# Kernel optimization log

Hardware: AMD Instinct MI355X
Metric: run time of the kernel (lower is better)

Reference implementation:

```python
import jax, jax.numpy as jnp
import numpy as np

N_PEP, N_MHC, N_TCR = 20000, 5000, 100000
EMB, HID = 128, 256
E_PM, E_MT = 200000, 400000
B = 50000


def setup_inputs() -> dict:
    key = jax.random.key(0)
    ks = jax.random.split(key, 30)
    f32 = jnp.float32

    def w(k, shape, fan_in):
        # torch Linear default: U(-1/sqrt(fan_in), 1/sqrt(fan_in))
        lim = 1.0 / np.sqrt(fan_in)
        return jax.random.uniform(k, shape, dtype=f32, minval=-lim, maxval=lim)

    inp = {
        # embedding tables (learned params)
        "emb_pep": jax.random.normal(ks[0], (N_PEP, EMB), dtype=f32),
        "emb_mhc": jax.random.normal(ks[1], (N_MHC, EMB), dtype=f32),
        "emb_tcr": jax.random.normal(ks[2], (N_TCR, EMB), dtype=f32),
        # edge lists (src=edge_index[0], dst=edge_index[1])
        "src_pm": jax.random.randint(ks[3], (E_PM,), 0, N_PEP, dtype=jnp.int32),
        "dst_pm": jax.random.randint(ks[4], (E_PM,), 0, N_MHC, dtype=jnp.int32),
        "src_mt": jax.random.randint(ks[5], (E_MT,), 0, N_MHC, dtype=jnp.int32),
        "dst_mt": jax.random.randint(ks[6], (E_MT,), 0, N_TCR, dtype=jnp.int32),
        # triplet pack indices
        "pack_pep": jax.random.randint(ks[7], (B,), 0, N_PEP, dtype=jnp.int32),
        "pack_mhc": jax.random.randint(ks[8], (B,), 0, N_MHC, dtype=jnp.int32),
        "pack_tcr": jax.random.randint(ks[9], (B,), 0, N_TCR, dtype=jnp.int32),
        # SAGEConv params: Wl (aggregated neighbors, with bias), Wr (root, no bias)
        # layer 1: pep->mhc (src 128, dst 128); mhc->tcr (src 128, dst 128)
        "l1_pm_Wl": w(ks[10], (HID, EMB), EMB), "l1_pm_bl": w(ks[11], (HID,), EMB),
        "l1_pm_Wr": w(ks[12], (HID, EMB), EMB),
        "l1_mt_Wl": w(ks[13], (HID, EMB), EMB), "l1_mt_bl": w(ks[14], (HID,), EMB),
        "l1_mt_Wr": w(ks[15], (HID, EMB), EMB),
        # layer 2: pep->mhc (src 128, dst 256); mhc->tcr (src 256, dst 256)
        "l2_pm_Wl": w(ks[16], (HID, EMB), EMB), "l2_pm_bl": w(ks[17], (HID,), EMB),
        "l2_pm_Wr": w(ks[18], (HID, HID), HID),
        "l2_mt_Wl": w(ks[19], (HID, HID), HID), "l2_mt_bl": w(ks[20], (HID,), HID),
        "l2_mt_Wr": w(ks[21], (HID, HID), HID),
        # proj_pep and head MLP
        "proj_W": w(ks[22], (HID, EMB), EMB), "proj_b": w(ks[23], (HID,), EMB),
        "head_W1": w(ks[24], (HID, 3 * HID), 3 * HID), "head_b1": w(ks[25], (HID,), 3 * HID),
        "head_W2": w(ks[26], (1, HID), HID), "head_b2": w(ks[27], (1,), HID),
    }
    return inp


def _sage(x_src, x_dst, src, dst, Wl, bl, Wr, n_dst):
    # SAGEConv(mean): lin_l(mean_{j in N(i)} x_src[j]) + lin_r(x_dst[i])
    msg = jax.ops.segment_sum(x_src[src], dst, num_segments=n_dst)  # [n_dst, d_src]
    cnt = jax.ops.segment_sum(jnp.ones((src.shape[0],), x_src.dtype), dst, num_segments=n_dst)
    mean = msg / jnp.maximum(cnt, 1.0)[:, None]
    return mean @ Wl.T + bl + x_dst @ Wr.T


def reference(emb_pep, emb_mhc, emb_tcr,
              src_pm, dst_pm, src_mt, dst_mt,
              pack_pep, pack_mhc, pack_tcr,
              l1_pm_Wl, l1_pm_bl, l1_pm_Wr, l1_mt_Wl, l1_mt_bl, l1_mt_Wr,
              l2_pm_Wl, l2_pm_bl, l2_pm_Wr, l2_mt_Wl, l2_mt_bl, l2_mt_Wr,
              proj_W, proj_b, head_W1, head_b1, head_W2, head_b2):
    relu = jax.nn.relu
    # layer 1 (HeteroConv reads all relations from the same input dict)
    mhc1 = relu(_sage(emb_pep, emb_mhc, src_pm, dst_pm, l1_pm_Wl, l1_pm_bl, l1_pm_Wr, N_MHC))
    tcr1 = relu(_sage(emb_mhc, emb_tcr, src_mt, dst_mt, l1_mt_Wl, l1_mt_bl, l1_mt_Wr, N_TCR))
    # layer 2 ('pep' is never a destination, so it keeps its embedding)
    mhc2 = relu(_sage(emb_pep, mhc1, src_pm, dst_pm, l2_pm_Wl, l2_pm_bl, l2_pm_Wr, N_MHC))
    tcr2 = relu(_sage(mhc1, tcr1, src_mt, dst_mt, l2_mt_Wl, l2_mt_bl, l2_mt_Wr, N_TCR))
    # projections + triplet gather (dropout disabled: inference)
    hp = (emb_pep @ proj_W.T + proj_b)[pack_pep]  # [B, HID]
    hm = mhc2[pack_mhc]
    ht = tcr2[pack_tcr]
    z = jnp.concatenate([hp, hm, ht], axis=-1)  # [B, 3*HID]
    hidden = relu(z @ head_W1.T + head_b1)
    logits = hidden @ head_W2.T + head_b2
    return logits.squeeze(-1)
```

## Files before the change

kernel.cpp:

```cpp
#include <hip/hip_runtime.h>

constexpr int NPEP = 20000, NMHC = 5000, NTCR = 100000;
constexpr int EPM = 200000, EMT = 400000, BB = 50000;
constexpr int MAXU = 50000;

typedef __attribute__((ext_vector_type(8))) short bf16x8;
typedef __attribute__((ext_vector_type(4))) float f32x4;

__device__ inline ushort f2bf(float x) {
    union { float f; unsigned u; } v; v.f = x;
    unsigned r = (v.u + 0x7FFF + ((v.u >> 16) & 1)) >> 16;
    return (ushort)r;
}
__device__ inline float bf2f(ushort b) {
    union { unsigned u; float f; } t; t.u = ((unsigned)b) << 16; return t.f;
}
__device__ inline void bf2x2(unsigned u, float& a, float& b) {
    union { unsigned x; float f; } t1, t2;
    t1.x = u << 16; t2.x = u & 0xffff0000u;
    a = t1.f; b = t2.f;
}
__device__ inline ushort4 f4bf(float4 v) {
    return make_ushort4(f2bf(v.x), f2bf(v.y), f2bf(v.z), f2bf(v.w));
}

__global__ __launch_bounds__(256) void prep_kernel(
    int* __restrict__ ibz,
    const float4* __restrict__ emb_pep, ushort4* __restrict__ emb_pep_b,
    const float4* __restrict__ Wr1f, ushort4* __restrict__ Wr1_b,
    const float4* __restrict__ Wr2f, ushort4* __restrict__ Wr2_b,
    const float* __restrict__ head_W1, ushort4* __restrict__ W1b_b, ushort4* __restrict__ W1c_b,
    const float* __restrict__ l1_pm_Wl, const float* __restrict__ l1_pm_Wr,
    const float* __restrict__ l1_mt_Wl, ushort* __restrict__ Wcat1_b,
    const float* __restrict__ l2_pm_Wl, const float* __restrict__ l2_pm_Wr,
    const float* __restrict__ l2_mt_Wl, ushort* __restrict__ Wcat2_b,
    const float4* __restrict__ emb_mhc, ushort* __restrict__ Acat1,
    const float* __restrict__ proj_W, const float* __restrict__ proj_b,
    ushort* __restrict__ Wcomp_b, float* __restrict__ bp) {
    __shared__ float red[128];
    const int b = blockIdx.x, tid = threadIdx.x;
    if (b < 303) {
        int i = b * 256 + tid;
        if (i < 77500) ((int4*)ibz)[i] = make_int4(0, 0, 0, 0);
    } else if (b < 2803) {
        int i = (b - 303) * 256 + tid;
        if (i < 640000) emb_pep_b[i] = f4bf(emb_pep[i]);
    } else if (b < 2835) {
        int i = (b - 2803) * 256 + tid;
        if (i < 8192) Wr1_b[i] = f4bf(Wr1f[i]);
    } else if (b < 2899) {
        int i = (b - 2835) * 256 + tid;
        if (i < 16384) Wr2_b[i] = f4bf(Wr2f[i]);
    } else if (b < 2963) {
        int i = (b - 2899) * 256 + tid;
        if (i < 16384) {
            int n = i >> 6, k4 = (i & 63) * 4;
            float4 v = *(const float4*)(head_W1 + (size_t)n * 768 + 256 + k4);
            W1b_b[i] = f4bf(v);
        }
    } else if (b < 3027) {
        int i = (b - 2963) * 256 + tid;
        if (i < 16384) {
            int n = i >> 6, k4 = (i & 63) * 4;
            float4 v = *(const float4*)(head_W1 + (size_t)n * 768 + 512 + k4);
            W1c_b[i] = f4bf(v);
        }
    } else if (b < 3539) {
        int idx = (b - 3027) * 256 + tid;
        if (idx < 131072) {
            int r = idx >> 8, k = idx & 255;
            float v;
            if (r < 256) v = (k < 128) ? l1_pm_Wl[r * 128 + k] : l1_pm_Wr[r * 128 + (k - 128)];
            else         v = (k < 128) ? 0.f : l1_mt_Wl[(r - 256) * 128 + (k - 128)];
            Wcat1_b[idx] = f2bf(v);
        }
    } else if (b < 4307) {
        int idx = (b - 3539) * 256 + tid;
        if (idx < 196608) {
            int r = idx / 384, k = idx - r * 384;
            float v;
            if (r < 256) v = (k < 128) ? l2_pm_Wl[r * 128 + k] : l2_pm_Wr[r * 256 + (k - 128)];
            else         v = (k < 128) ? 0.f : l2_mt_Wl[(r - 256) * 256 + (k - 128)];
            Wcat2_b[idx] = f2bf(v);
        }
    } else if (b < 4932) {
        int i4 = (b - 4307) * 256 + tid;
        if (i4 < 160000) {
            int r = i4 >> 5, c4 = (i4 & 31) * 4;
            *(ushort4*)(Acat1 + (size_t)r * 256 + 128 + c4) = f4bf(emb_mhc[i4]);
        }
    } else {
        int i = b - 4932;
        const float* w1row = head_W1 + (size_t)i * 768;
        if (tid < 128) {
            float acc = 0.f;
            for (int k = 0; k < 256; k++) acc += w1row[k] * proj_W[k * 128 + tid];
            Wcomp_b[i * 128 + tid] = f2bf(acc);
            float pb = w1row[2 * tid] * proj_b[2 * tid] + w1row[2 * tid + 1] * proj_b[2 * tid + 1];
            red[tid] = pb;
        }
        __syncthreads();
        if (tid < 64) { red[tid] += red[tid + 64]; }
        __syncthreads();
        if (tid < 32) { red[tid] += red[tid + 32]; }
        __syncthreads();
        if (tid == 0) {
            float s = 0.f;
            for (int j = 0; j < 32; j++) s += red[j];
            bp[i] = s;
        }
    }
}

__global__ void hist2_kernel(const int* __restrict__ dst_pm, const int* __restrict__ dst_mt,
                             const int* __restrict__ pack_tcr,
                             int* __restrict__ deg_pm, int* __restrict__ deg_mt,
                             int* __restrict__ mark) {
    int t = blockIdx.x * blockDim.x + threadIdx.x;
    if (t < EPM) atomicAdd(&deg_pm[dst_pm[t]], 1);
    else if (t < EPM + EMT) atomicAdd(&deg_mt[dst_mt[t - EPM]], 1);
    else if (t < EPM + EMT + BB) mark[pack_tcr[t - EPM - EMT]] = 1;
}

__global__ __launch_bounds__(256) void blocksum2_kernel(const int* __restrict__ deg_pm,
                                                        const int* __restrict__ deg_mt,
                                                        const int* __restrict__ mark,
                                                        int* __restrict__ bsum_pm,
                                                        int* __restrict__ bsum_mt,
                                                        int* __restrict__ bsum_mk) {
    __shared__ int red[256];
    const int tid = threadIdx.x;
    const int* deg; int n, bi; int* bsum;
    if (blockIdx.x < 5) { deg = deg_pm; n = NMHC; bi = blockIdx.x; bsum = bsum_pm; }
    else if (blockIdx.x < 103) { deg = deg_mt; n = NTCR; bi = blockIdx.x - 5; bsum = bsum_mt; }
    else { deg = mark; n = NTCR; bi = blockIdx.x - 103; bsum = bsum_mk; }
    const int base = bi * 1024;
    int s = 0;
#pragma unroll
    for (int j = 0; j < 4; j++) {
        int i = base + tid + j * 256;
        if (i < n) s += deg[i];
    }
    red[tid] = s;
    __syncthreads();
    for (int off = 128; off > 0; off >>= 1) {
        if (tid < off) red[tid] += red[tid + off];
        __syncthreads();
    }
    if (tid == 0) bsum[bi] = red[0];
}

__global__ __launch_bounds__(128) void scanb2_kernel(int* __restrict__ bsum_pm,
                                                     int* __restrict__ bsum_mt,
                                                     int* __restrict__ bsum_mk) {
    __shared__ int s[128];
    const int tid = threadIdx.x;
    int* bsum = (blockIdx.x == 0) ? bsum_pm : ((blockIdx.x == 1) ? bsum_mt : bsum_mk);
    const int nb = (blockIdx.x == 0) ? 5 : 98;
    int v = (tid < nb) ? bsum[tid] : 0;
    s[tid] = v;
    __syncthreads();
    for (int off = 1; off < 128; off <<= 1) {
        int t = (tid >= off) ? s[tid - off] : 0;
        __syncthreads();
        s[tid] += t;
        __syncthreads();
    }
    if (tid < nb) bsum[tid] = (tid > 0) ? s[tid - 1] : 0;
    if (tid == 0) bsum[nb] = s[nb - 1];
}

__global__ __launch_bounds__(256) void emit2_kernel(const int* __restrict__ deg_pm,
                                                    const int* __restrict__ deg_mt,
                                                    const int* __restrict__ mark,
                                                    const int* __restrict__ bsum_pm,
                                                    const int* __restrict__ bsum_mt,
                                                    const int* __restrict__ bsum_mk,
                                                    int* __restrict__ rp_pm, float* __restrict__ cnt_pm,
                                                    int* __restrict__ rp_mt, float* __restrict__ cnt_mt,
                                                    int* __restrict__ list) {
    __shared__ int tsum[256];
    const int tid = threadIdx.x;
    const int* deg; const int* bsum; int* rp; float* cnt; int n, nb, bi, mode;
    if (blockIdx.x < 5) { deg = deg_pm; bsum = bsum_pm; rp = rp_pm; cnt = cnt_pm; n = NMHC; nb = 5; bi = blockIdx.x; mode = 0; }
    else if (blockIdx.x < 103) { deg = deg_mt; bsum = bsum_mt; rp = rp_mt; cnt = cnt_mt; n = NTCR; nb = 98; bi = blockIdx.x - 5; mode = 0; }
    else { deg = mark; bsum = bsum_mk; rp = nullptr; cnt = nullptr; n = NTCR; nb = 98; bi = blockIdx.x - 103; mode = 1; }
    const int i0 = bi * 1024 + tid * 4;
    int4 v = make_int4(0, 0, 0, 0);
    if (i0 + 3 < n) v = *(const int4*)(deg + i0);
    else if (i0 < n) {
        int t[4] = {0, 0, 0, 0};
        for (int j = 0; j < 4 && i0 + j < n; j++) t[j] = deg[i0 + j];
        v = make_int4(t[0], t[1], t[2], t[3]);
    }
    int s = v.x + v.y + v.z + v.w;
    tsum[tid] = s;
    __syncthreads();
    for (int off = 1; off < 256; off <<= 1) {
        int t = (tid >= off) ? tsum[tid - off] : 0;
        __syncthreads();
        tsum[tid] += t;
        __syncthreads();
    }
    int ex = ((tid > 0) ? tsum[tid - 1] : 0) + bsum[bi];
    if (mode == 0) {
        if (i0 + 3 < n) {
            int r1 = ex + v.x, r2 = r1 + v.y, r3 = r2 + v.z;
            *(int4*)(rp + i0) = make_int4(ex, r1, r2, r3);
            *(float4*)(cnt + i0) = make_float4((float)v.x, (float)v.y, (float)v.z, (float)v.w);
        } else if (i0 < n) {
            int r = ex;
            int vv[4] = {v.x, v.y, v.z, v.w};
            for (int j = 0; j < 4 && i0 + j < n; j++) {
                rp[i0 + j] = r;
                cnt[i0 + j] = (float)vv[j];
                r += vv[j];
            }
        }
        if (bi == 0 && tid == 0) rp[n] = bsum[nb];
    } else {
        int p = ex;
        int vv[4] = {v.x, v.y, v.z, v.w};
#pragma unroll
        for (int j = 0; j < 4; j++) {
            if (i0 + j < n && vv[j]) list[p++] = i0 + j;
        }
    }
}

__global__ void fill2_kernel(const int* __restrict__ src_pm, const int* __restrict__ dst_pm,
                             const int* __restrict__ src_mt, const int* __restrict__ dst_mt,
                             const int* __restrict__ rp_pm, int* __restrict__ cur_pm, int* __restrict__ csr_pm,
                             const int* __restrict__ rp_mt, int* __restrict__ cur_mt, int* __restrict__ csr_mt) {
    int t = blockIdx.x * blockDim.x + threadIdx.x;
    if (t < EPM) {
        int d = dst_pm[t];
        int pos = atomicAdd(&cur_pm[d], 1);
        csr_pm[rp_pm[d] + pos] = src_pm[t];
    } else if (t < EPM + EMT) {
        int t2 = t - EPM;
        int d = dst_mt[t2];
        int pos = atomicAdd(&cur_mt[d], 1);
        csr_mt[rp_mt[d] + pos] = src_mt[t2];
    }
}

__global__ __launch_bounds__(256) void gatherpm_kernel(const int* __restrict__ rp,
                                                       const int* __restrict__ csr_src,
                                                       const float* __restrict__ X,
                                                       ushort* __restrict__ A1, ushort* __restrict__ A2,
                                                       int n) {
    const int tid = threadIdx.x;
    const int r = blockIdx.x * 8 + (tid >> 5);
    const int lane = tid & 31;
    if (r >= n) return;
    const int e0 = rp[r], e1 = rp[r + 1];
    float4 s = make_float4(0.f, 0.f, 0.f, 0.f);
    for (int e = e0; e < e1; e++) {
        const int sidx = csr_src[e];
        float4 v = ((const float4*)(X + (long)sidx * 128))[lane];
        s.x += v.x; s.y += v.y; s.z += v.z; s.w += v.w;
    }
    float sc = 1.f / fmaxf((float)(e1 - e0), 1.f);
    ushort4 o = make_ushort4(f2bf(s.x * sc), f2bf(s.y * sc), f2bf(s.z * sc), f2bf(s.w * sc));
    *(ushort4*)(A1 + (size_t)r * 256 + lane * 4) = o;
    *(ushort4*)(A2 + (size_t)r * 384 + lane * 4) = o;
}

__global__ __launch_bounds__(256) void gatherb2_kernel(const int* __restrict__ rp,
                                                       const int* __restrict__ csr_src,
                                                       const ushort* __restrict__ Z1,
                                                       const ushort* __restrict__ Z2,
                                                       const int* __restrict__ list,
                                                       const int* __restrict__ nrowsp,
                                                       float* __restrict__ cntc,
                                                       ushort* __restrict__ a1,
                                                       ushort* __restrict__ a2) {
    const int tid = threadIdx.x;
    const int r = blockIdx.x * 8 + (tid >> 5);
    const int lane = tid & 31;
    const int nrows = nrowsp[0];
    if (r >= nrows) return;
    const int orig = list[r];
    const int e0 = rp[orig], e1 = rp[orig + 1];
    if (lane == 0) cntc[r] = (float)(e1 - e0);
    float s1[8] = {}, s2[8] = {};
    for (int e = e0; e < e1; e++) {
        const int sidx = csr_src[e];
        uint4 u1 = *(const uint4*)(Z1 + (size_t)sidx * 256 + lane * 8);
        uint4 u2 = *(const uint4*)(Z2 + (size_t)sidx * 256 + lane * 8);
        float a, b;
        bf2x2(u1.x, a, b); s1[0] += a; s1[1] += b;
        bf2x2(u1.y, a, b); s1[2] += a; s1[3] += b;
        bf2x2(u1.z, a, b); s1[4] += a; s1[5] += b;
        bf2x2(u1.w, a, b); s1[6] += a; s1[7] += b;
        bf2x2(u2.x, a, b); s2[0] += a; s2[1] += b;
        bf2x2(u2.y, a, b); s2[2] += a; s2[3] += b;
        bf2x2(u2.z, a, b); s2[4] += a; s2[5] += b;
        bf2x2(u2.w, a, b); s2[6] += a; s2[7] += b;
    }
    uint4 w1, w2;
    w1.x = (unsigned)f2bf(s1[0]) | ((unsigned)f2bf(s1[1]) << 16);
    w1.y = (unsigned)f2bf(s1[2]) | ((unsigned)f2bf(s1[3]) << 16);
    w1.z = (unsigned)f2bf(s1[4]) | ((unsigned)f2bf(s1[5]) << 16);
    w1.w = (unsigned)f2bf(s1[6]) | ((unsigned)f2bf(s1[7]) << 16);
    w2.x = (unsigned)f2bf(s2[0]) | ((unsigned)f2bf(s2[1]) << 16);
    w2.y = (unsigned)f2bf(s2[2]) | ((unsigned)f2bf(s2[3]) << 16);
    w2.z = (unsigned)f2bf(s2[4]) | ((unsigned)f2bf(s2[5]) << 16);
    w2.w = (unsigned)f2bf(s2[6]) | ((unsigned)f2bf(s2[7]) << 16);
    *(uint4*)(a1 + (size_t)r * 256 + lane * 8) = w1;
    *(uint4*)(a2 + (size_t)r * 256 + lane * 8) = w2;
}

template <int K, int NB0, bool RELU0, bool G2>
__global__ __launch_bounds__(256, 2) void mfma_fused_kernel(
    int M, const ushort* __restrict__ A, const ushort* __restrict__ W,
    const float* __restrict__ bias,
    ushort* __restrict__ out0, int s0, ushort* __restrict__ out1) {
    constexpr int RS = 40;
    __shared__ ushort Als[128 * RS];
    __shared__ ushort Wls[128 * RS];
    const int tid = threadIdx.x;
    const int m0 = blockIdx.x * 128, n0 = blockIdx.y * 128;
    const int lane = tid & 63, w = tid >> 6;
    const int wm = w >> 1, wn = w & 1;
    const int m16 = lane & 15, q = lane >> 4;

    f32x4 acc[4][4] = {};

    for (int k0 = 0; k0 < K; k0 += 32) {
        bf16x8 a_st[2], w_st[2];
#pragma unroll
        for (int r = 0; r < 2; r++) {
            int chunk = tid + r * 256;
            int row = chunk >> 2, off = (chunk & 3) * 8;
            int ga = min(m0 + row, M - 1);
            a_st[r] = *(const bf16x8*)(A + (size_t)ga * K + k0 + off);
            w_st[r] = *(const bf16x8*)(W + (size_t)(n0 + row) * K + k0 + off);
        }
        __syncthreads();
#pragma unroll
        for (int r = 0; r < 2; r++) {
            int chunk = tid + r * 256;
            int row = chunk >> 2, off = (chunk & 3) * 8;
            *(bf16x8*)(&Als[row * RS + off]) = a_st[r];
            *(bf16x8*)(&Wls[row * RS + off]) = w_st[r];
        }
        __syncthreads();
        bf16x8 af[4], bf[4];
#pragma unroll
        for (int t = 0; t < 4; t++) {
            af[t] = *(const bf16x8*)(&Als[(wm * 64 + t * 16 + m16) * RS + q * 8]);
            bf[t] = *(const bf16x8*)(&Wls[(wn * 64 + t * 16 + m16) * RS + q * 8]);
        }
#pragma unroll
        for (int mt = 0; mt < 4; mt++)
#pragma unroll
            for (int nt = 0; nt < 4; nt++)
                acc[mt][nt] = __builtin_amdgcn_mfma_f32_16x16x32_bf16(af[mt], bf[nt], acc[mt][nt], 0, 0, 0);
    }

    const bool g1 = G2 && ((int)blockIdx.y >= NB0);
#pragma unroll
    for (int mt = 0; mt < 4; mt++) {
#pragma unroll
        for (int i = 0; i < 4; i++) {
            int row = m0 + wm * 64 + mt * 16 + q * 4 + i;
            if (row >= M) continue;
#pragma unroll
            for (int nt = 0; nt < 4; nt++) {
                int col = n0 + wn * 64 + nt * 16 + m16;
                float v = acc[mt][nt][i];
                if (!g1) {
                    v += bias[col];
                    if (RELU0) v = fmaxf(v, 0.f);
                    out0[(size_t)row * s0 + col] = f2bf(v);
                } else {
                    out1[(size_t)row * 256 + (col - NB0 * 128)] = f2bf(v);
                }
            }
        }
    }
}

__global__ __launch_bounds__(256, 4) void tcrall_kernel(
    const int* __restrict__ nrowsp, const int* __restrict__ list,
    const float* __restrict__ emb_tcr,
    const ushort* __restrict__ Wr1, const ushort* __restrict__ Wr2,
    const ushort* __restrict__ W1c,
    const float* __restrict__ bl1, const float* __restrict__ bl2,
    const float* __restrict__ cnt,
    const ushort* __restrict__ acc1, const ushort* __restrict__ acc2,
    ushort* __restrict__ Ht) {
    constexpr int RS1 = 136;
    constexpr int RS2 = 264;
    __shared__ ushort B[32 * RS2];
    __shared__ int origs[32];
    const int tid = threadIdx.x;
    const int M = nrowsp[0];
    const int m0 = blockIdx.x * 32;
    if (m0 >= M) return;
    const int lane = tid & 63, w = tid >> 6;
    const int m16 = lane & 15, q = lane >> 4;

    if (tid < 32) origs[tid] = list[min(m0 + tid, M - 1)];

#pragma unroll
    for (int r = 0; r < 4; r++) {
        int chunk = tid + r * 256;
        int row = chunk >> 5, c4 = (chunk & 31) * 4;
        int grow = list[min(m0 + row, M - 1)];
        float4 v = *(const float4*)(emb_tcr + (size_t)grow * 128 + c4);
        *(ushort4*)(&B[row * RS1 + c4]) = f4bf(v);
    }
    __syncthreads();

    {
        f32x4 acc[2][4] = {};
        for (int k0 = 0; k0 < 128; k0 += 32) {
            bf16x8 af[2], bf[4];
#pragma unroll
            for (int t = 0; t < 2; t++)
                af[t] = *(const bf16x8*)(&B[(t * 16 + m16) * RS1 + k0 + q * 8]);
#pragma unroll
            for (int t = 0; t < 4; t++)
                bf[t] = *(const bf16x8*)(Wr1 + (size_t)(w * 64 + t * 16 + m16) * 128 + k0 + q * 8);
#pragma unroll
            for (int mt = 0; mt < 2; mt++)
#pragma unroll
                for (int nt = 0; nt < 4; nt++)
                    acc[mt][nt] = __builtin_amdgcn_mfma_f32_16x16x32_bf16(af[mt], bf[nt], acc[mt][nt], 0, 0, 0);
        }
        __syncthreads();
#pragma unroll
        for (int mt = 0; mt < 2; mt++)
#pragma unroll
            for (int i = 0; i < 4; i++) {
                int lr = mt * 16 + q * 4 + i;
                int rc = min(m0 + lr, M - 1);
                float es = 1.f / fmaxf(cnt[rc], 1.f);
#pragma unroll
                for (int nt = 0; nt < 4; nt++) {
                    int col = w * 64 + nt * 16 + m16;
                    float v = acc[mt][nt][i] + bl1[col] + bf2f(acc1[(size_t)rc * 256 + col]) * es;
                    B[lr * RS2 + col] = f2bf(fmaxf(v, 0.f));
                }
            }
    }
    __syncthreads();

    {
        f32x4 acc[2][4] = {};
        for (int k0 = 0; k0 < 256; k0 += 32) {
            bf16x8 af[2], bf[4];
#pragma unroll
            for (int t = 0; t < 2; t++)
                af[t] = *(const bf16x8*)(&B[(t * 16 + m16) * RS2 + k0 + q * 8]);
#pragma unroll
            for (int t = 0; t < 4; t++)
                bf[t] = *(const bf16x8*)(Wr2 + (size_t)(w * 64 + t * 16 + m16) * 256 + k0 + q * 8);
#pragma unroll
            for (int mt = 0; mt < 2; mt++)
#pragma unroll
                for (int nt = 0; nt < 4; nt++)
                    acc[mt][nt] = __builtin_amdgcn_mfma_f32_16x16x32_bf16(af[mt], bf[nt], acc[mt][nt], 0, 0, 0);
        }
        __syncthreads();
#pragma unroll
        for (int mt = 0; mt < 2; mt++)
#pragma unroll
            for (int i = 0; i < 4; i++) {
                int lr = mt * 16 + q * 4 + i;
                int rc = min(m0 + lr, M - 1);
                float es = 1.f / fmaxf(cnt[rc], 1.f);
#pragma unroll
                for (int nt = 0; nt < 4; nt++) {
                    int col = w * 64 + nt * 16 + m16;
                    float v = acc[mt][nt][i] + bl2[col] + bf2f(acc2[(size_t)rc * 256 + col]) * es;
                    B[lr * RS2 + col] = f2bf(fmaxf(v, 0.f));
                }
            }
    }
    __syncthreads();

    {
        f32x4 acc[2][4] = {};
        for (int k0 = 0; k0 < 256; k0 += 32) {
            bf16x8 af[2], bf[4];
#pragma unroll
            for (int t = 0; t < 2; t++)
                af[t] = *(const bf16x8*)(&B[(t * 16 + m16) * RS2 + k0 + q * 8]);
#pragma unroll
            for (int t = 0; t < 4; t++)
                bf[t] = *(const bf16x8*)(W1c + (size_t)(w * 64 + t * 16 + m16) * 256 + k0 + q * 8);
#pragma unroll
            for (int mt = 0; mt < 2; mt++)
#pragma unroll
                for (int nt = 0; nt < 4; nt++)
                    acc[mt][nt] = __builtin_amdgcn_mfma_f32_16x16x32_bf16(af[mt], bf[nt], acc[mt][nt], 0, 0, 0);
        }
        __syncthreads();
#pragma unroll
        for (int mt = 0; mt < 2; mt++)
#pragma unroll
            for (int i = 0; i < 4; i++) {
                int lr = mt * 16 + q * 4 + i;
#pragma unroll
                for (int nt = 0; nt < 4; nt++) {
                    int col = w * 64 + nt * 16 + m16;
                    B[lr * RS2 + col] = f2bf(acc[mt][nt][i]);
                }
            }
    }
    __syncthreads();

#pragma unroll
    for (int r = 0; r < 4; r++) {
        int chunk = tid + r * 256;
        int row = chunk >> 5, c8 = (chunk & 31) * 8;
        if (m0 + row < M)
            *(uint4*)(Ht + (size_t)origs[row] * 256 + c8) = *(const uint4*)(&B[row * RS2 + c8]);
    }
}

template <int K, bool HASB>
__global__ __launch_bounds__(256, 2) void mfma_out_kernel(
    int M, const ushort* __restrict__ A, const ushort* __restrict__ W,
    const float* __restrict__ bias, ushort* __restrict__ out) {
    constexpr int RS = 40;
    __shared__ ushort Als[128 * RS];
    __shared__ ushort Wls[128 * RS];
    const int tid = threadIdx.x;
    const int m0 = blockIdx.x * 128, n0 = blockIdx.y * 128;
    const int lane = tid & 63, w = tid >> 6;
    const int wm = w >> 1, wn = w & 1;
    const int m16 = lane & 15, q = lane >> 4;

    f32x4 acc[4][4] = {};

    for (int k0 = 0; k0 < K; k0 += 32) {
        bf16x8 a_st[2], w_st[2];
#pragma unroll
        for (int r = 0; r < 2; r++) {
            int chunk = tid + r * 256;
            int row = chunk >> 2, off = (chunk & 3) * 8;
            int ga = min(m0 + row, M - 1);
            a_st[r] = *(const bf16x8*)(A + (size_t)ga * K + k0 + off);
            w_st[r] = *(const bf16x8*)(W + (size_t)(n0 + row) * K + k0 + off);
        }
        __syncthreads();
#pragma unroll
        for (int r = 0; r < 2; r++) {
            int chunk = tid + r * 256;
            int row = chunk >> 2, off = (chunk & 3) * 8;
            *(bf16x8*)(&Als[row * RS + off]) = a_st[r];
            *(bf16x8*)(&Wls[row * RS + off]) = w_st[r];
        }
        __syncthreads();
        bf16x8 af[4], bf[4];
#pragma unroll
        for (int t = 0; t < 4; t++) {
            af[t] = *(const bf16x8*)(&Als[(wm * 64 + t * 16 + m16) * RS + q * 8]);
            bf[t] = *(const bf16x8*)(&Wls[(wn * 64 + t * 16 + m16) * RS + q * 8]);
        }
#pragma unroll
        for (int mt = 0; mt < 4; mt++)
#pragma unroll
            for (int nt = 0; nt < 4; nt++)
                acc[mt][nt] = __builtin_amdgcn_mfma_f32_16x16x32_bf16(af[mt], bf[nt], acc[mt][nt], 0, 0, 0);
    }

#pragma unroll
    for (int mt = 0; mt < 4; mt++) {
#pragma unroll
        for (int i = 0; i < 4; i++) {
            int row = m0 + wm * 64 + mt * 16 + q * 4 + i;
            if (row >= M) continue;
#pragma unroll
            for (int nt = 0; nt < 4; nt++) {
                int col = n0 + wn * 64 + nt * 16 + m16;
                float v = acc[mt][nt][i];
                if (HASB) v += bias[col];
                out[(size_t)row * 256 + col] = f2bf(v);
            }
        }
    }
}

__global__ __launch_bounds__(256) void combine_kernel(
    const ushort* __restrict__ Hp, const ushort* __restrict__ Hm, const ushort* __restrict__ Ht,
    const int* __restrict__ pp, const int* __restrict__ pm, const int* __restrict__ pt,
    const float* __restrict__ b1, const float* __restrict__ W2, const float* __restrict__ b2,
    float* __restrict__ out) {
    const int tid = threadIdx.x;
    const int lane = tid & 63, w = tid >> 6;
    const int c = lane * 4;
    const float4 b1v = *(const float4*)(b1 + c);
    const float4 w2v = *(const float4*)(W2 + c);
    const float b2v = b2[0];
    const int base = blockIdx.x * 32 + w * 8;
#pragma unroll
    for (int t = 0; t < 8; t++) {
        int i = base + t;
        if (i >= BB) return;
        int ra = pp[i], rb = pm[i], rc = pt[i];
        ushort4 ua = *(const ushort4*)(Hp + (size_t)ra * 256 + c);
        ushort4 ub = *(const ushort4*)(Hm + (size_t)rb * 256 + c);
        ushort4 uc = *(const ushort4*)(Ht + (size_t)rc * 256 + c);
        float h0 = fmaxf(bf2f(ua.x) + bf2f(ub.x) + bf2f(uc.x) + b1v.x, 0.f);
        float h1 = fmaxf(bf2f(ua.y) + bf2f(ub.y) + bf2f(uc.y) + b1v.y, 0.f);
        float h2 = fmaxf(bf2f(ua.z) + bf2f(ub.z) + bf2f(uc.z) + b1v.z, 0.f);
        float h3 = fmaxf(bf2f(ua.w) + bf2f(ub.w) + bf2f(uc.w) + b1v.w, 0.f);
        float p = h0 * w2v.x + h1 * w2v.y + h2 * w2v.z + h3 * w2v.w;
#pragma unroll
        for (int off = 32; off > 0; off >>= 1) p += __shfl_down(p, off);
        if (lane == 0) out[i] = p + b2v;
    }
}

extern "C" void kernel_launch(void* const* d_in, const int* in_sizes, int n_in,
                              void* d_out, int out_size, void* d_ws, size_t ws_size,
                              hipStream_t stream) {
    const float* emb_pep = (const float*)d_in[0];
    const float* emb_mhc = (const float*)d_in[1];
    const float* emb_tcr = (const float*)d_in[2];
    const int* src_pm = (const int*)d_in[3];
    const int* dst_pm = (const int*)d_in[4];
    const int* src_mt = (const int*)d_in[5];
    const int* dst_mt = (const int*)d_in[6];
    const int* pack_pep = (const int*)d_in[7];
    const int* pack_mhc = (const int*)d_in[8];
    const int* pack_tcr = (const int*)d_in[9];
    const float* l1_pm_Wl = (const float*)d_in[10];
    const float* l1_pm_bl = (const float*)d_in[11];
    const float* l1_pm_Wr = (const float*)d_in[12];
    const float* l1_mt_Wl = (const float*)d_in[13];
    const float* l1_mt_bl = (const float*)d_in[14];
    const float* l1_mt_Wr = (const float*)d_in[15];
    const float* l2_pm_Wl = (const float*)d_in[16];
    const float* l2_pm_bl = (const float*)d_in[17];
    const float* l2_pm_Wr = (const float*)d_in[18];
    const float* l2_mt_Wl = (const float*)d_in[19];
    const float* l2_mt_bl = (const float*)d_in[20];
    const float* l2_mt_Wr = (const float*)d_in[21];
    const float* proj_W = (const float*)d_in[22];
    const float* proj_b = (const float*)d_in[23];
    const float* head_W1 = (const float*)d_in[24];
    const float* head_b1 = (const float*)d_in[25];
    const float* head_W2 = (const float*)d_in[26];
    const float* head_b2 = (const float*)d_in[27];
    float* out = (float*)d_out;

    int* ib = (int*)d_ws;
    int* deg_pm = ib;
    int* cur_pm = ib + 5000;
    int* deg_mt = ib + 10000;
    int* cur_mt = ib + 110000;
    int* mark   = ib + 210000;
    int* rp_pm  = ib + 310000;
    int* rp_mt  = ib + 315008;
    int* csr_pm = ib + 415016;
    int* csr_mt = ib + 615016;
    int* bsum_pm = ib + 1015016;
    int* bsum_mt = ib + 1015176;
    int* bsum_mk = ib + 1015336;
    int* list    = ib + 1015496;

    float* f = (float*)(ib + 1065544);
    float* cnt_pm = f;
    float* cnt_mt = f + 5000;
    float* cntc   = f + 105000;
    float* bp     = f + 155000;

    ushort* u = (ushort*)(f + 155264);
    ushort* Wcat1_b = u;
    ushort* Wcat2_b = u + 131072;
    ushort* W1b_b   = u + 327680;
    ushort* W1c_b   = u + 393216;
    ushort* Wcomp_b = u + 458752;
    ushort* Wr1_b   = u + 491520;
    ushort* Wr2_b   = u + 524288;
    ushort* Acat1   = u + 589824;
    ushort* Acat2   = u + 1869824;
    ushort* Zb1     = u + 3789824;
    ushort* Zb2     = u + 5069824;
    ushort* mhc2_b  = u + 6349824;
    ushort* emb_pep_b = u + 7629824;
    ushort* Hp_b    = u + 10189824;
    ushort* Hm_b    = u + 15309824;
    ushort* acc1_c  = u + 16589824;
    ushort* acc2_c  = u + 29389824;
    ushort* Ht_b    = u + 42189824;

    prep_kernel<<<5188, 256, 0, stream>>>(
        ib,
        (const float4*)emb_pep, (ushort4*)emb_pep_b,
        (const float4*)l1_mt_Wr, (ushort4*)Wr1_b,
        (const float4*)l2_mt_Wr, (ushort4*)Wr2_b,
        head_W1, (ushort4*)W1b_b, (ushort4*)W1c_b,
        l1_pm_Wl, l1_pm_Wr, l1_mt_Wl, Wcat1_b,
        l2_pm_Wl, l2_pm_Wr, l2_mt_Wl, Wcat2_b,
        (const float4*)emb_mhc, Acat1,
        proj_W, proj_b, Wcomp_b, bp);

    hist2_kernel<<<(EPM + EMT + BB + 255) / 256, 256, 0, stream>>>(
        dst_pm, dst_mt, pack_tcr, deg_pm, deg_mt, mark);
    blocksum2_kernel<<<201, 256, 0, stream>>>(deg_pm, deg_mt, mark, bsum_pm, bsum_mt, bsum_mk);
    scanb2_kernel<<<3, 128, 0, stream>>>(bsum_pm, bsum_mt, bsum_mk);
    emit2_kernel<<<201, 256, 0, stream>>>(deg_pm, deg_mt, mark, bsum_pm, bsum_mt, bsum_mk,
                                          rp_pm, cnt_pm, rp_mt, cnt_mt, list);
    fill2_kernel<<<(EPM + EMT + 255) / 256, 256, 0, stream>>>(
        src_pm, dst_pm, src_mt, dst_mt, rp_pm, cur_pm, csr_pm, rp_mt, cur_mt, csr_mt);

    gatherpm_kernel<<<(NMHC + 7) / 8, 256, 0, stream>>>(rp_pm, csr_pm, emb_pep, Acat1, Acat2, NMHC);

    mfma_fused_kernel<256, 2, true, true><<<dim3((NMHC + 127) / 128, 4), 256, 0, stream>>>(
        NMHC, Acat1, Wcat1_b, l1_pm_bl, Acat2 + 128, 384, Zb1);
    mfma_fused_kernel<384, 2, true, true><<<dim3((NMHC + 127) / 128, 4), 256, 0, stream>>>(
        NMHC, Acat2, Wcat2_b, l2_pm_bl, mhc2_b, 256, Zb2);

    gatherb2_kernel<<<(MAXU + 7) / 8, 256, 0, stream>>>(
        rp_mt, csr_mt, Zb1, Zb2, list, bsum_mk + 98, cntc, acc1_c, acc2_c);

    tcrall_kernel<<<(MAXU + 31) / 32, 256, 0, stream>>>(
        bsum_mk + 98, list, emb_tcr, Wr1_b, Wr2_b, W1c_b,
        l1_mt_bl, l2_mt_bl, cntc, acc1_c, acc2_c, Ht_b);

    mfma_out_kernel<128, true><<<dim3((NPEP + 127) / 128, 2), 256, 0, stream>>>(
        NPEP, emb_pep_b, Wcomp_b, bp, Hp_b);
    mfma_out_kernel<256, false><<<dim3((NMHC + 127) / 128, 2), 256, 0, stream>>>(
        NMHC, mhc2_b, W1b_b, nullptr, Hm_b);

    combine_kernel<<<(BB + 31) / 32, 256, 0, stream>>>(
        Hp_b, Hm_b, Ht_b, pack_pep, pack_mhc, pack_tcr,
        head_b1, head_W2, head_b2, out);
}
```

Measured before the change: 419.1 us.

## Fuse TCR neighbor gather into tcrall kernel and convert emb_pep on the fly

Removes the separate gatherb2 kernel: each tcrall block now aggregates the mean of Z1/Z2 neighbor rows for its 32 TCR rows directly into shared memory, so the bf16 intermediate buffers are no longer written to and read back from global memory. It also drops the prep-stage fp32-to-bf16 copy of emb_pep and has the projection GEMM convert fp32 inputs while loading tiles. The extra shared memory lowers occupancy (launch bounds from 4 to 3), and the irregular gather now runs inside the GEMM kernel, where load imbalance can stall the block.

Result: no change. 416.3 us (-0.7%).

```diff
diff --git a/kernel.cpp b/kernel.cpp
--- a/kernel.cpp
+++ b/kernel.cpp
@@ -26,7 +26,6 @@
 
 __global__ __launch_bounds__(256) void prep_kernel(
     int* __restrict__ ibz,
-    const float4* __restrict__ emb_pep, ushort4* __restrict__ emb_pep_b,
     const float4* __restrict__ Wr1f, ushort4* __restrict__ Wr1_b,
     const float4* __restrict__ Wr2f, ushort4* __restrict__ Wr2_b,
     const float* __restrict__ head_W1, ushort4* __restrict__ W1b_b, ushort4* __restrict__ W1c_b,
@@ -42,31 +41,28 @@
     if (b < 303) {
         int i = b * 256 + tid;
         if (i < 77500) ((int4*)ibz)[i] = make_int4(0, 0, 0, 0);
-    } else if (b < 2803) {
+    } else if (b < 335) {
         int i = (b - 303) * 256 + tid;
-        if (i < 640000) emb_pep_b[i] = f4bf(emb_pep[i]);
-    } else if (b < 2835) {
-        int i = (b - 2803) * 256 + tid;
         if (i < 8192) Wr1_b[i] = f4bf(Wr1f[i]);
-    } else if (b < 2899) {
-        int i = (b - 2835) * 256 + tid;
+    } else if (b < 399) {
+        int i = (b - 335) * 256 + tid;
         if (i < 16384) Wr2_b[i] = f4bf(Wr2f[i]);
-    } else if (b < 2963) {
-        int i = (b - 2899) * 256 + tid;
+    } else if (b < 463) {
+        int i = (b - 399) * 256 + tid;
         if (i < 16384) {
             int n = i >> 6, k4 = (i & 63) * 4;
             float4 v = *(const float4*)(head_W1 + (size_t)n * 768 + 256 + k4);
             W1b_b[i] = f4bf(v);
         }
-    } else if (b < 3027) {
-        int i = (b - 2963) * 256 + tid;
+    } else if (b < 527) {
+        int i = (b - 463) * 256 + tid;
         if (i < 16384) {
             int n = i >> 6, k4 = (i & 63) * 4;
             float4 v = *(const float4*)(head_W1 + (size_t)n * 768 + 512 + k4);
             W1c_b[i] = f4bf(v);
         }
-    } else if (b < 3539) {
-        int idx = (b - 3027) * 256 + tid;
+    } else if (b < 1039) {
+        int idx = (b - 527) * 256 + tid;
         if (idx < 131072) {
             int r = idx >> 8, k = idx & 255;
             float v;
@@ -74,8 +70,8 @@
             else         v = (k < 128) ? 0.f : l1_mt_Wl[(r - 256) * 128 + (k - 128)];
             Wcat1_b[idx] = f2bf(v);
         }
-    } else if (b < 4307) {
-        int idx = (b - 3539) * 256 + tid;
+    } else if (b < 1807) {
+        int idx = (b - 1039) * 256 + tid;
         if (idx < 196608) {
             int r = idx / 384, k = idx - r * 384;
             float v;
@@ -83,14 +79,14 @@
             else         v = (k < 128) ? 0.f : l2_mt_Wl[(r - 256) * 256 + (k - 128)];
             Wcat2_b[idx] = f2bf(v);
         }
-    } else if (b < 4932) {
-        int i4 = (b - 4307) * 256 + tid;
+    } else if (b < 2432) {
+        int i4 = (b - 1807) * 256 + tid;
         if (i4 < 160000) {
             int r = i4 >> 5, c4 = (i4 & 31) * 4;
             *(ushort4*)(Acat1 + (size_t)r * 256 + 128 + c4) = f4bf(emb_mhc[i4]);
         }
     } else {
-        int i = b - 4932;
+        int i = b - 2432;
         const float* w1row = head_W1 + (size_t)i * 768;
         if (tid < 128) {
             float acc = 0.f;
@@ -267,51 +263,6 @@
     *(ushort4*)(A2 + (size_t)r * 384 + lane * 4) = o;
 }
 
-__global__ __launch_bounds__(256) void gatherb2_kernel(const int* __restrict__ rp,
-                                                       const int* __restrict__ csr_src,
-                                                       const ushort* __restrict__ Z1,
-                                                       const ushort* __restrict__ Z2,
-                                                       const int* __restrict__ list,
-                                                       const int* __restrict__ nrowsp,
-                                                       float* __restrict__ cntc,
-                                                       ushort* __restrict__ a1,
-                                                       ushort* __restrict__ a2) {
-    const int tid = threadIdx.x;
-    const int r = blockIdx.x * 8 + (tid >> 5);
-    const int lane = tid & 31;
-    const int nrows = nrowsp[0];
-    if (r >= nrows) return;
-    const int orig = list[r];
-    const int e0 = rp[orig], e1 = rp[orig + 1];
-    if (lane == 0) cntc[r] = (float)(e1 - e0);
-    float s1[8] = {}, s2[8] = {};
-    for (int e = e0; e < e1; e++) {
-        const int sidx = csr_src[e];
-        uint4 u1 = *(const uint4*)(Z1 + (size_t)sidx * 256 + lane * 8);
-        uint4 u2 = *(const uint4*)(Z2 + (size_t)sidx * 256 + lane * 8);
-        float a, b;
-        bf2x2(u1.x, a, b); s1[0] += a; s1[1] += b;
-        bf2x2(u1.y, a, b); s1[2] += a; s1[3] += b;
-        bf2x2(u1.z, a, b); s1[4] += a; s1[5] += b;
-        bf2x2(u1.w, a, b); s1[6] += a; s1[7] += b;
-        bf2x2(u2.x, a, b); s2[0] += a; s2[1] += b;
-        bf2x2(u2.y, a, b); s2[2] += a; s2[3] += b;
-        bf2x2(u2.z, a, b); s2[4] += a; s2[5] += b;
-        bf2x2(u2.w, a, b); s2[6] += a; s2[7] += b;
-    }
-    uint4 w1, w2;
-    w1.x = (unsigned)f2bf(s1[0]) | ((unsigned)f2bf(s1[1]) << 16);
-    w1.y = (unsigned)f2bf(s1[2]) | ((unsigned)f2bf(s1[3]) << 16);
-    w1.z = (unsigned)f2bf(s1[4]) | ((unsigned)f2bf(s1[5]) << 16);
-    w1.w = (unsigned)f2bf(s1[6]) | ((unsigned)f2bf(s1[7]) << 16);
-    w2.x = (unsigned)f2bf(s2[0]) | ((unsigned)f2bf(s2[1]) << 16);
-    w2.y = (unsigned)f2bf(s2[2]) | ((unsigned)f2bf(s2[3]) << 16);
-    w2.z = (unsigned)f2bf(s2[4]) | ((unsigned)f2bf(s2[5]) << 16);
-    w2.w = (unsigned)f2bf(s2[6]) | ((unsigned)f2bf(s2[7]) << 16);
-    *(uint4*)(a1 + (size_t)r * 256 + lane * 8) = w1;
-    *(uint4*)(a2 + (size_t)r * 256 + lane * 8) = w2;
-}
-
 template <int K, int NB0, bool RELU0, bool G2>
 __global__ __launch_bounds__(256, 2) void mfma_fused_kernel(
     int M, const ushort* __restrict__ A, const ushort* __restrict__ W,
@@ -383,18 +334,20 @@
     }
 }
 
-__global__ __launch_bounds__(256, 4) void tcrall_kernel(
+__global__ __launch_bounds__(256, 3) void tcrall_kernel(
     const int* __restrict__ nrowsp, const int* __restrict__ list,
+    const int* __restrict__ rp, const int* __restrict__ csr_src,
+    const ushort* __restrict__ Z1, const ushort* __restrict__ Z2,
     const float* __restrict__ emb_tcr,
     const ushort* __restrict__ Wr1, const ushort* __restrict__ Wr2,
     const ushort* __restrict__ W1c,
     const float* __restrict__ bl1, const float* __restrict__ bl2,
-    const float* __restrict__ cnt,
-    const ushort* __restrict__ acc1, const ushort* __restrict__ acc2,
     ushort* __restrict__ Ht) {
     constexpr int RS1 = 136;
     constexpr int RS2 = 264;
     __shared__ ushort B[32 * RS2];
+    __shared__ ushort A1[32 * RS2];
+    __shared__ ushort A2[32 * RS2];
     __shared__ int origs[32];
     const int tid = threadIdx.x;
     const int M = nrowsp[0];
@@ -413,6 +366,42 @@
         float4 v = *(const float4*)(emb_tcr + (size_t)grow * 128 + c4);
         *(ushort4*)(&B[row * RS1 + c4]) = f4bf(v);
     }
+
+    {
+        const int g = tid >> 5, gl = tid & 31;
+        for (int rr = g; rr < 32; rr += 8) {
+            int cr = min(m0 + rr, M - 1);
+            int orig = list[cr];
+            int e0 = rp[orig], e1 = rp[orig + 1];
+            float s1[8] = {}, s2[8] = {};
+            for (int e = e0; e < e1; e++) {
+                int sidx = csr_src[e];
+                uint4 u1 = *(const uint4*)(Z1 + (size_t)sidx * 256 + gl * 8);
+                uint4 u2 = *(const uint4*)(Z2 + (size_t)sidx * 256 + gl * 8);
+                float a, b;
+                bf2x2(u1.x, a, b); s1[0] += a; s1[1] += b;
+                bf2x2(u1.y, a, b); s1[2] += a; s1[3] += b;
+                bf2x2(u1.z, a, b); s1[4] += a; s1[5] += b;
+                bf2x2(u1.w, a, b); s1[6] += a; s1[7] += b;
+                bf2x2(u2.x, a, b); s2[0] += a; s2[1] += b;
+                bf2x2(u2.y, a, b); s2[2] += a; s2[3] += b;
+                bf2x2(u2.z, a, b); s2[4] += a; s2[5] += b;
+                bf2x2(u2.w, a, b); s2[6] += a; s2[7] += b;
+            }
+            float es = 1.f / fmaxf((float)(e1 - e0), 1.f);
+            uint4 w1, w2;
+            w1.x = (unsigned)f2bf(s1[0] * es) | ((unsigned)f2bf(s1[1] * es) << 16);
+            w1.y = (unsigned)f2bf(s1[2] * es) | ((unsigned)f2bf(s1[3] * es) << 16);
+            w1.z = (unsigned)f2bf(s1[4] * es) | ((unsigned)f2bf(s1[5] * es) << 16);
+            w1.w = (unsigned)f2bf(s1[6] * es) | ((unsigned)f2bf(s1[7] * es) << 16);
+            w2.x = (unsigned)f2bf(s2[0] * es) | ((unsigned)f2bf(s2[1] * es) << 16);
+            w2.y = (unsigned)f2bf(s2[2] * es) | ((unsigned)f2bf(s2[3] * es) << 16);
+            w2.z = (unsigned)f2bf(s2[4] * es) | ((unsigned)f2bf(s2[5] * es) << 16);
+            w2.w = (unsigned)f2bf(s2[6] * es) | ((unsigned)f2bf(s2[7] * es) << 16);
+            *(uint4*)(&A1[rr * RS2 + gl * 8]) = w1;
+            *(uint4*)(&A2[rr * RS2 + gl * 8]) = w2;
+        }
+    }
     __syncthreads();
 
     {
@@ -437,12 +426,10 @@
 #pragma unroll
             for (int i = 0; i < 4; i++) {
                 int lr = mt * 16 + q * 4 + i;
-                int rc = min(m0 + lr, M - 1);
-                float es = 1.f / fmaxf(cnt[rc], 1.f);
 #pragma unroll
                 for (int nt = 0; nt < 4; nt++) {
                     int col = w * 64 + nt * 16 + m16;
-                    float v = acc[mt][nt][i] + bl1[col] + bf2f(acc1[(size_t)rc * 256 + col]) * es;
+                    float v = acc[mt][nt][i] + bl1[col] + bf2f(A1[lr * RS2 + col]);
                     B[lr * RS2 + col] = f2bf(fmaxf(v, 0.f));
                 }
             }
@@ -471,12 +458,10 @@
 #pragma unroll
             for (int i = 0; i < 4; i++) {
                 int lr = mt * 16 + q * 4 + i;
-                int rc = min(m0 + lr, M - 1);
-                float es = 1.f / fmaxf(cnt[rc], 1.f);
 #pragma unroll
                 for (int nt = 0; nt < 4; nt++) {
                     int col = w * 64 + nt * 16 + m16;
-                    float v = acc[mt][nt][i] + bl2[col] + bf2f(acc2[(size_t)rc * 256 + col]) * es;
+                    float v = acc[mt][nt][i] + bl2[col] + bf2f(A2[lr * RS2 + col]);
                     B[lr * RS2 + col] = f2bf(fmaxf(v, 0.f));
                 }
             }
@@ -523,9 +508,9 @@
     }
 }
 
-template <int K, bool HASB>
+template <int K, bool HASB, bool AF32>
 __global__ __launch_bounds__(256, 2) void mfma_out_kernel(
-    int M, const ushort* __restrict__ A, const ushort* __restrict__ W,
+    int M, const void* __restrict__ Av, const ushort* __restrict__ W,
     const float* __restrict__ bias, ushort* __restrict__ out) {
     constexpr int RS = 40;
     __shared__ ushort Als[128 * RS];
@@ -545,7 +530,18 @@
             int chunk = tid + r * 256;
             int row = chunk >> 2, off = (chunk & 3) * 8;
             int ga = min(m0 + row, M - 1);
-            a_st[r] = *(const bf16x8*)(A + (size_t)ga * K + k0 + off);
+            if constexpr (AF32) {
+                const float* Af = (const float*)Av;
+                float4 f0 = *(const float4*)(Af + (size_t)ga * K + k0 + off);
+                float4 f1 = *(const float4*)(Af + (size_t)ga * K + k0 + off + 4);
+                ushort4 u0 = f4bf(f0), u1 = f4bf(f1);
+                bf16x8 av;
+                av[0] = (short)u0.x; av[1] = (short)u0.y; av[2] = (short)u0.z; av[3] = (short)u0.w;
+                av[4] = (short)u1.x; av[5] = (short)u1.y; av[6] = (short)u1.z; av[7] = (short)u1.w;
+                a_st[r] = av;
+            } else {
+                a_st[r] = *(const bf16x8*)((const ushort*)Av + (size_t)ga * K + k0 + off);
+            }
             w_st[r] = *(const bf16x8*)(W + (size_t)(n0 + row) * K + k0 + off);
         }
         __syncthreads();
@@ -669,10 +665,9 @@
     float* f = (float*)(ib + 1065544);
     float* cnt_pm = f;
     float* cnt_mt = f + 5000;
-    float* cntc   = f + 105000;
-    float* bp     = f + 155000;
-
-    ushort* u = (ushort*)(f + 155264);
+    float* bp     = f + 105000;
+
+    ushort* u = (ushort*)(f + 105344);
     ushort* Wcat1_b = u;
     ushort* Wcat2_b = u + 131072;
     ushort* W1b_b   = u + 327680;
@@ -685,16 +680,12 @@
     ushort* Zb1     = u + 3789824;
     ushort* Zb2     = u + 5069824;
     ushort* mhc2_b  = u + 6349824;
-    ushort* emb_pep_b = u + 7629824;
-    ushort* Hp_b    = u + 10189824;
-    ushort* Hm_b    = u + 15309824;
-    ushort* acc1_c  = u + 16589824;
-    ushort* acc2_c  = u + 29389824;
-    ushort* Ht_b    = u + 42189824;
-
-    prep_kernel<<<5188, 256, 0, stream>>>(
+    ushort* Hp_b    = u + 7629824;
+    ushort* Hm_b    = u + 12749824;
+    ushort* Ht_b    = u + 14029824;
+
+    prep_kernel<<<2688, 256, 0, stream>>>(
         ib,
-        (const float4*)emb_pep, (ushort4*)emb_pep_b,
         (const float4*)l1_mt_Wr, (ushort4*)Wr1_b,
         (const float4*)l2_mt_Wr, (ushort4*)Wr2_b,
         head_W1, (ushort4*)W1b_b, (ushort4*)W1c_b,
@@ -719,16 +710,13 @@
     mfma_fused_kernel<384, 2, true, true><<<dim3((NMHC + 127) / 128, 4), 256, 0, stream>>>(
         NMHC, Acat2, Wcat2_b, l2_pm_bl, mhc2_b, 256, Zb2);
 
-    gatherb2_kernel<<<(MAXU + 7) / 8, 256, 0, stream>>>(
-        rp_mt, csr_mt, Zb1, Zb2, list, bsum_mk + 98, cntc, acc1_c, acc2_c);
-
     tcrall_kernel<<<(MAXU + 31) / 32, 256, 0, stream>>>(
-        bsum_mk + 98, list, emb_tcr, Wr1_b, Wr2_b, W1c_b,
-        l1_mt_bl, l2_mt_bl, cntc, acc1_c, acc2_c, Ht_b);
-
-    mfma_out_kernel<128, true><<<dim3((NPEP + 127) / 128, 2), 256, 0, stream>>>(
-        NPEP, emb_pep_b, Wcomp_b, bp, Hp_b);
-    mfma_out_kernel<256, false><<<dim3((NMHC + 127) / 128, 2), 256, 0, stream>>>(
+        bsum_mk + 98, list, rp_mt, csr_mt, Zb1, Zb2, emb_tcr,
+        Wr1_b, Wr2_b, W1c_b, l1_mt_bl, l2_mt_bl, Ht_b);
+
+    mfma_out_kernel<128, true, true><<<dim3((NPEP + 127) / 128, 2), 256, 0, stream>>>(
+        NPEP, emb_pep, Wcomp_b, bp, Hp_b);
+    mfma_out_kernel<256, false, false><<<dim3((NMHC + 127) / 128, 2), 256, 0, stream>>>(
         NMHC, mhc2_b, W1b_b, nullptr, Hm_b);
 
     combine_kernel<<<(BB + 31) / 32, 256, 0, stream>>>(
```
